# Kernel tuning notes

Measured on AMD Instinct MI355X. Metric: run time of the kernel, lower is better.

## Reference

```python
import jax, jax.numpy as jnp
import numpy as np

P = 16      # patch size
D = 768     # d_model
H = 12      # heads
L = 12      # layers
F = 3072    # d_ff
NC = 1000   # num classes
B = 32
IMG = 224
S = (IMG // P) ** 2 + 1  # 197 tokens (CLS + patches)
EPS = 1e-5


def layernorm(x, s, b):
    m = jnp.mean(x, axis=-1, keepdims=True)
    v = jnp.var(x, axis=-1, keepdims=True)
    return (x - m) * jax.lax.rsqrt(v + EPS) * s + b


def setup_inputs() -> dict:
    key = jax.random.key(0)
    ks = jax.random.split(key, 16)
    sd = 0.02
    patch_dim = P * P * 3  # 768
    inp = {
        "img": jax.random.normal(ks[0], (B, 3, IMG, IMG), jnp.float32),
        "proj_w": jax.random.normal(ks[1], (patch_dim, D), jnp.float32) * sd,
        "proj_b": jnp.zeros((D,), jnp.float32),
        "cls_token": jax.random.normal(ks[2], (1, 1, D), jnp.float32) * sd,
        "pos_emb": jax.random.normal(ks[3], (1, S, D), jnp.float32) * sd,
        # stacked per-layer params [L, ...]
        "ln1_s": jnp.ones((L, D), jnp.float32),
        "ln1_b": jnp.zeros((L, D), jnp.float32),
        "wq": jax.random.normal(ks[4], (L, D, D), jnp.float32) * sd,
        "bq": jnp.zeros((L, D), jnp.float32),
        "wk": jax.random.normal(ks[5], (L, D, D), jnp.float32) * sd,
        "bk": jnp.zeros((L, D), jnp.float32),
        "wv": jax.random.normal(ks[6], (L, D, D), jnp.float32) * sd,
        "bv": jnp.zeros((L, D), jnp.float32),
        "wo": jax.random.normal(ks[7], (L, D, D), jnp.float32) * sd,
        "bo": jnp.zeros((L, D), jnp.float32),
        "ln2_s": jnp.ones((L, D), jnp.float32),
        "ln2_b": jnp.zeros((L, D), jnp.float32),
        "w1": jax.random.normal(ks[8], (L, D, F), jnp.float32) * sd,
        "b1": jnp.zeros((L, F), jnp.float32),
        "w2": jax.random.normal(ks[9], (L, F, D), jnp.float32) * sd,
        "b2": jnp.zeros((L, D), jnp.float32),
        "fnorm_s": jnp.ones((D,), jnp.float32),
        "fnorm_b": jnp.zeros((D,), jnp.float32),
        "head_w": jax.random.normal(ks[10], (D, NC), jnp.float32) * sd,
        "head_b": jnp.zeros((NC,), jnp.float32),
    }
    return inp


def vit_forward(img, proj_w, proj_b, cls_token, pos_emb, ln1_s, ln1_b,
                wq, bq, wk, bk, wv, bv, wo, bo, ln2_s, ln2_b,
                w1, b1, w2, b2, fnorm_s, fnorm_b, head_w, head_b):
    b = img.shape[0]
    g = IMG // P
    # rearrange 'b c (h ph) (w pw) -> b (h w) (ph pw c)'
    x = img.reshape(b, 3, g, P, g, P)
    x = x.transpose(0, 2, 4, 3, 5, 1).reshape(b, g * g, P * P * 3)
    x = x @ proj_w + proj_b                      # [b, 196, D]
    cls = jnp.broadcast_to(cls_token, (b, 1, D))
    x = jnp.concatenate([cls, x], axis=1)        # [b, 197, D]
    x = x + pos_emb                              # learnable positional encoding

    dk = D // H
    scale = 1.0 / jnp.sqrt(jnp.float32(dk))

    def layer(x, p):
        (l1s, l1b, Wq, Bq, Wk, Bk, Wv, Bv, Wo, Bo,
         l2s, l2b, W1, B1, W2, B2) = p
        # pre-norm self-attention with residual
        xn = layernorm(x, l1s, l1b)
        q = (xn @ Wq + Bq).reshape(b, S, H, dk)
        k = (xn @ Wk + Bk).reshape(b, S, H, dk)
        v = (xn @ Wv + Bv).reshape(b, S, H, dk)
        scores = jnp.einsum('bqhd,bkhd->bhqk', q, k) * scale
        attn = jax.nn.softmax(scores, axis=-1)
        ao = jnp.einsum('bhqk,bkhd->bqhd', attn, v).reshape(b, S, D)
        x = x + (ao @ Wo + Bo)
        # pre-norm FFN with residual
        xn = layernorm(x, l2s, l2b)
        h = jax.nn.gelu(xn @ W1 + B1, approximate=False)
        x = x + (h @ W2 + B2)
        return x, None

    params = (ln1_s, ln1_b, wq, bq, wk, bk, wv, bv, wo, bo,
              ln2_s, ln2_b, w1, b1, w2, b2)
    x, _ = jax.lax.scan(layer, x, params)
    x = layernorm(x, fnorm_s, fnorm_b)
    cls_out = x[:, 0, :]
    return cls_out @ head_w + head_b             # [b, num_classes]


def reference(img, proj_w, proj_b, cls_token, pos_emb, ln1_s, ln1_b,
              wq, bq, wk, bk, wv, bv, wo, bo, ln2_s, ln2_b,
              w1, b1, w2, b2, fnorm_s, fnorm_b, head_w, head_b):
    return vit_forward(img, proj_w, proj_b, cls_token, pos_emb, ln1_s, ln1_b,
                       wq, bq, wk, bk, wv, bv, wo, bo, ln2_s, ln2_b,
                       w1, b1, w2, b2, fnorm_s, fnorm_b, head_w, head_b)
```

## Files before the change

### kernel.cpp

```cpp
#include <hip/hip_runtime.h>
#include <stdint.h>

typedef __attribute__((ext_vector_type(4))) float  f32x4;
typedef __attribute__((ext_vector_type(8))) _Float16 f16x8;
typedef __attribute__((ext_vector_type(8))) unsigned short u16x8;

__device__ __forceinline__ unsigned short f2h(float f) {
    _Float16 h = (_Float16)f;
    union { _Float16 h; unsigned short u; } cv; cv.h = h; return cv.u;
}

__device__ __forceinline__ f32x4 mfma16(f16x8 a, f16x8 b, f32x4 c) {
    return __builtin_amdgcn_mfma_f32_16x16x32_f16(a, b, c, 0, 0, 0);
}

__device__ __forceinline__ void async16(const unsigned short* g, unsigned short* l) {
    __builtin_amdgcn_global_load_lds(
        (const __attribute__((address_space(1))) unsigned int*)g,
        (__attribute__((address_space(3))) unsigned int*)l,
        16, 0, 0);
}

template<int EPI, int BK>
__global__ __launch_bounds__(256, (BK == 32 ? 4 : 3))
void gemm_k(const unsigned short* __restrict__ A, const unsigned short* __restrict__ Bw,
            int M, int K, int N,
            float* __restrict__ p0, unsigned short* __restrict__ p1,
            const float* __restrict__ p2, const float* __restrict__ p3,
            unsigned short* __restrict__ p4, unsigned short* __restrict__ p5)
{
    constexpr int SMSTG = 2 * 64 * BK + 2 * 128 * BK;
    constexpr int SMU   = (EPI == 0 || EPI == 2)
                          ? (SMSTG > 128 * 68 ? SMSTG : 128 * 68)
                          : SMSTG;
    __shared__ unsigned short smem[SMU];
    unsigned short (*lA)[64 * BK]  = (unsigned short(*)[64 * BK])smem;
    unsigned short (*lB)[128 * BK] = (unsigned short(*)[128 * BK])(smem + 2 * 64 * BK);
    const int tid  = threadIdx.x;
    const int lane = tid & 63;
    const int wid  = tid >> 6;

    const int gx  = gridDim.x;
    const int nwg = gx * gridDim.y;
    const int lin = blockIdx.y * gx + blockIdx.x;
    const int q = nwg >> 3, r = nwg & 7;
    const int xcd = lin & 7, i = lin >> 3;
    const int wg  = (xcd < r ? xcd * (q + 1) : r * (q + 1) + (xcd - r) * q) + i;
    const int m0 = (wg / gx) * 64;
    const int n0 = (wg % gx) * 128;

    const int colBase = wid * 32;
    const int fr = lane & 15, fg = lane >> 4;

    f32x4 acc[4][2];
#pragma unroll
    for (int a = 0; a < 4; ++a)
#pragma unroll
        for (int b = 0; b < 2; ++b) acc[a][b] = (f32x4){0.f, 0.f, 0.f, 0.f};

    const int nk = K / BK;
    constexpr int CPR = BK / 8;
    constexpr int ACH = 64 * CPR;
    constexpr int NH  = (ACH + 128 * CPR) / 256;

    auto stage = [&](int buf, int kt) {
        const int k0 = kt * BK;
#pragma unroll
        for (int h = 0; h < NH; ++h) {
            const int c = h * 256 + tid;
            const int wbase = h * 256 + wid * 64;
            if (c < ACH) {
                const int row = c / CPR, kc = c % CPR;
                const int gkc = (BK == 32) ? (kc ^ ((row >> 1) & 3)) : (kc ^ (row & 7));
                int ar = m0 + row; if (ar > M - 1) ar = M - 1;
                async16(A + (size_t)ar * K + k0 + gkc * 8,
                        &lA[buf][(size_t)wbase * 8]);
            } else {
                const int cb = c - ACH;
                const int row = cb / CPR, kc = cb % CPR;
                const int gkc = (BK == 32) ? (kc ^ ((row >> 1) & 3)) : (kc ^ (row & 7));
                async16(Bw + (size_t)(n0 + row) * K + k0 + gkc * 8,
                        &lB[buf][(size_t)(wbase - ACH) * 8]);
            }
        }
    };

    stage(0, 0);
    for (int kt = 0; kt < nk; ++kt) {
        __syncthreads();
        if (kt + 1 < nk) stage((kt + 1) & 1, kt + 1);
        const int buf = kt & 1;
#pragma unroll
        for (int kk = 0; kk < BK / 32; ++kk) {
            f16x8 af[4], bfv[2];
#pragma unroll
            for (int mi = 0; mi < 4; ++mi) {
                int row = mi * 16 + fr;
                int pc  = (BK == 32) ? (fg ^ ((row >> 1) & 3))
                                     : ((kk * 4 + fg) ^ (row & 7));
                af[mi] = *(const f16x8*)(&lA[buf][row * BK + pc * 8]);
            }
#pragma unroll
            for (int ni = 0; ni < 2; ++ni) {
                int row = colBase + ni * 16 + fr;
                int pc  = (BK == 32) ? (fg ^ ((row >> 1) & 3))
                                     : ((kk * 4 + fg) ^ (row & 7));
                bfv[ni] = *(const f16x8*)(&lB[buf][row * BK + pc * 8]);
            }
#pragma unroll
            for (int mi = 0; mi < 4; ++mi)
#pragma unroll
                for (int ni = 0; ni < 2; ++ni)
                    acc[mi][ni] = mfma16(af[mi], bfv[ni], acc[mi][ni]);
        }
    }

    const int mat0 = (EPI == 0) ? (n0 / 768) : 0;

    if constexpr (EPI == 0 || EPI == 2) {
        if (EPI == 2 || mat0 < 2) {
            unsigned short* sm = smem;
            __syncthreads();
#pragma unroll
            for (int mi = 0; mi < 4; ++mi)
#pragma unroll
                for (int ni = 0; ni < 2; ++ni) {
                    const int lcol = colBase + ni * 16 + fr;
                    const int colg = n0 + lcol;
#pragma unroll
                    for (int reg = 0; reg < 4; ++reg) {
                        const int lrow = mi * 16 + fg * 4 + reg;
                        float val = acc[mi][ni][reg] + p2[colg];
                        if (EPI == 2)
                            val = 0.5f * val * (1.0f + erff(val * 0.70710678118654752f));
                        sm[lrow * 136 + lcol] = f2h(val);
                    }
                }
            __syncthreads();
#pragma unroll
            for (int it = 0; it < 4; ++it) {
                const int e = it * 256 + tid;
                const int lrow = e >> 4, cch = e & 15;
                const int grow = m0 + lrow;
                if (grow >= M) continue;
                const u16x8 v = *(const u16x8*)(&sm[lrow * 136 + cch * 8]);
                if (EPI == 2) {
                    *(u16x8*)(p1 + (size_t)grow * 3072 + n0 + cch * 8) = v;
                } else {
                    const int colg = n0 + cch * 8;
                    const int w = colg - mat0 * 768;
                    const int h = w >> 6, d = w & 63;
                    const int b = grow / 197, s = grow - b * 197;
                    unsigned short* dst = (mat0 == 0) ? p1 : p4;
                    *(u16x8*)(dst + ((((size_t)b * 12 + h) * 197 + s) * 64 + d)) = v;
                }
            }
        } else {
            unsigned short* sm = smem;
            __syncthreads();
#pragma unroll
            for (int mi = 0; mi < 4; ++mi)
#pragma unroll
                for (int ni = 0; ni < 2; ++ni) {
                    const int lcol = colBase + ni * 16 + fr;
                    const int colg = n0 + lcol;
#pragma unroll
                    for (int reg = 0; reg < 4; ++reg) {
                        const int lrow = mi * 16 + fg * 4 + reg;
                        sm[lcol * 68 + lrow] = f2h(acc[mi][ni][reg] + p2[colg]);
                    }
                }
            __syncthreads();
            const int srow = lane;
            const int grow = m0 + srow;
            if (grow < M) {
                const int b = grow / 197, s = grow - b * 197;
#pragma unroll
                for (int it = 0; it < 32; ++it) {
                    const int c = (tid >> 6) + it * 4;
                    const int w = n0 + c - 1536;
                    const int h = w >> 6, d = w & 63;
                    p5[(((size_t)b * 12 + h) * 64 + d) * 208 + s] = sm[c * 68 + srow];
                }
            }
        }
    } else {
#pragma unroll
        for (int mi = 0; mi < 4; ++mi) {
#pragma unroll
            for (int ni = 0; ni < 2; ++ni) {
                const int col = n0 + colBase + ni * 16 + fr;
#pragma unroll
                for (int reg = 0; reg < 4; ++reg) {
                    const int row = m0 + mi * 16 + fg * 4 + reg;
                    if (row >= M) continue;
                    const float v = acc[mi][ni][reg];
                    if constexpr (EPI == 1 || EPI == 3) {
                        size_t idx = (size_t)row * 768 + col;
                        p0[idx] = p0[idx] + v + p2[col];
                    } else {
                        int b = row / 196, p = row - b * 196;
                        float val = v + p2[col] + p3[(size_t)(1 + p) * 768 + col];
                        p0[((size_t)(b * 197 + 1 + p)) * 768 + col] = val;
                    }
                }
            }
        }
    }
}

__device__ __forceinline__ void convT_body(const float* __restrict__ src,
                                           unsigned short* __restrict__ dst,
                                           int K, int N, int bx, int by,
                                           float (*t)[65])
{
    const int tid = threadIdx.x;
    const int n0 = bx * 64, k0 = by * 64;
    int r = tid >> 4, cq = tid & 15;
#pragma unroll
    for (int i = 0; i < 4; ++i) {
        f32x4 v = *(const f32x4*)(src + (size_t)(k0 + r + i * 16) * N + n0 + cq * 4);
        t[r + i * 16][cq * 4 + 0] = v.x;
        t[r + i * 16][cq * 4 + 1] = v.y;
        t[r + i * 16][cq * 4 + 2] = v.z;
        t[r + i * 16][cq * 4 + 3] = v.w;
    }
    __syncthreads();
    int nl = tid >> 2, kq = tid & 3;
    u16x8 o0, o1;
#pragma unroll
    for (int j = 0; j < 8; ++j) {
        o0[j] = f2h(t[kq * 16 + j][nl]);
        o1[j] = f2h(t[kq * 16 + 8 + j][nl]);
    }
    unsigned short* d = dst + (size_t)(n0 + nl) * K + k0 + kq * 16;
    *(u16x8*)(d)     = o0;
    *(u16x8*)(d + 8) = o1;
}

__device__ __forceinline__ void prep_block(int pid,
            const float* __restrict__ wq, const float* __restrict__ wk,
            const float* __restrict__ wv, const float* __restrict__ wo,
            const float* __restrict__ w1, const float* __restrict__ w2,
            const float* __restrict__ bq, const float* __restrict__ bk,
            const float* __restrict__ bv,
            unsigned short* __restrict__ wqkvT, unsigned short* __restrict__ woT,
            unsigned short* __restrict__ w1T, unsigned short* __restrict__ w2T,
            float* __restrict__ bqkv, float (*t)[65])
{
    if (pid == 1728) {
        for (int c = threadIdx.x; c < 2304; c += 256) {
            int m = c / 768, w = c - m * 768;
            bqkv[c] = (m == 0) ? bq[w] : (m == 1 ? bk[w] : bv[w]);
        }
        return;
    }
    const float* src; unsigned short* dst; int K, N, bx, by;
    if (pid < 576) {
        int mat = pid / 144, r = pid - mat * 144;
        K = 768; N = 768; bx = r % 12; by = r / 12;
        if (mat == 0)      { src = wq; dst = wqkvT; }
        else if (mat == 1) { src = wk; dst = wqkvT + 768ull * 768; }
        else if (mat == 2) { src = wv; dst = wqkvT + 1536ull * 768; }
        else               { src = wo; dst = woT; }
    } else if (pid < 1152) {
        int r = pid - 576; K = 768; N = 3072; bx = r % 48; by = r / 48;
        src = w1; dst = w1T;
    } else {
        int r = pid - 1152; K = 3072; N = 768; bx = r % 12; by = r / 12;
        src = w2; dst = w2T;
    }
    convT_body(src, dst, K, N, bx, by, t);
}

__global__ __launch_bounds__(256)
void prep_k(const float* __restrict__ wq, const float* __restrict__ wk,
            const float* __restrict__ wv, const float* __restrict__ wo,
            const float* __restrict__ w1, const float* __restrict__ w2,
            const float* __restrict__ bq, const float* __restrict__ bk,
            const float* __restrict__ bv,
            unsigned short* __restrict__ wqkvT, unsigned short* __restrict__ woT,
            unsigned short* __restrict__ w1T, unsigned short* __restrict__ w2T,
            float* __restrict__ bqkv)
{
    __shared__ float t[64][65];
    prep_block(blockIdx.x, wq, wk, wv, wo, w1, w2, bq, bk, bv,
               wqkvT, woT, w1T, w2T, bqkv, t);
}

__global__ __launch_bounds__(256, 4)
void attn_prep_k(const unsigned short* __restrict__ qb, const unsigned short* __restrict__ kb,
                 const unsigned short* __restrict__ vt, unsigned short* __restrict__ ao,
                 const float* __restrict__ wq, const float* __restrict__ wk,
                 const float* __restrict__ wv, const float* __restrict__ wo,
                 const float* __restrict__ w1, const float* __restrict__ w2,
                 const float* __restrict__ bq, const float* __restrict__ bk,
                 const float* __restrict__ bv,
                 unsigned short* __restrict__ wqkvT, unsigned short* __restrict__ woT,
                 unsigned short* __restrict__ w1T, unsigned short* __restrict__ w2T,
                 float* __restrict__ bqkv)
{
    __shared__ float smbuf[32 * 210 + 32];

    const int bid = blockIdx.x;
    if (bid >= 2688) {
        prep_block(bid - 2688, wq, wk, wv, wo, w1, w2, bq, bk, bv,
                   wqkvT, woT, w1T, w2T, bqkv,
                   reinterpret_cast<float(*)[65]>(smbuf));
        return;
    }

    float* sc   = smbuf;
    float* rinv = smbuf + 32 * 210;

    const int bh = bid % 384;
    const int qt = bid / 384;
    const int b = bh / 12, h = bh - b * 12;
    const unsigned short* qh  = qb + (size_t)bh * 197 * 64;
    const unsigned short* kh  = kb + (size_t)bh * 197 * 64;
    const unsigned short* vth = vt + (size_t)bh * 64 * 208;
    const int tid = threadIdx.x, lane = tid & 63, wid = tid >> 6;
    const int fr = lane & 15, fg = lane >> 4;

    f16x8 qf[2][2];
#pragma unroll
    for (int mi = 0; mi < 2; ++mi)
#pragma unroll
        for (int kc = 0; kc < 2; ++kc) {
            int s = qt * 32 + mi * 16 + fr; if (s > 196) s = 196;
            qf[mi][kc] = *(const f16x8*)(qh + (size_t)s * 64 + kc * 32 + fg * 8);
        }

    for (int nt = wid; nt < 13; nt += 4) {
        f32x4 a0 = (f32x4){0.f,0.f,0.f,0.f}, a1 = a0;
        int rs = nt * 16 + fr; if (rs > 196) rs = 196;
#pragma unroll
        for (int kc = 0; kc < 2; ++kc) {
            f16x8 kf = *(const f16x8*)(kh + (size_t)rs * 64 + kc * 32 + fg * 8);
            a0 = mfma16(qf[0][kc], kf, a0);
            a1 = mfma16(qf[1][kc], kf, a1);
        }
        int ccol = nt * 16 + fr;
        bool valid = (ccol < 197);
#pragma unroll
        for (int reg = 0; reg < 4; ++reg) {
            int mr = fg * 4 + reg;
            sc[mr * 210 + ccol]        = valid ? a0[reg] * 0.125f : -1e30f;
            sc[(16 + mr) * 210 + ccol] = valid ? a1[reg] * 0.125f : -1e30f;
        }
    }
    __syncthreads();

    {
        int row = tid >> 3, j = tid & 7;
        float m = -1e30f;
        for (int c = j; c < 208; c += 8) m = fmaxf(m, sc[row * 210 + c]);
#pragma unroll
        for (int o = 1; o < 8; o <<= 1) m = fmaxf(m, __shfl_xor(m, o));
        float sum = 0.f;
        for (int c = j; c < 208; c += 8) {
            float e = __expf(sc[row * 210 + c] - m);
            sc[row * 210 + c] = e;
            sum += e;
        }
#pragma unroll
        for (int o = 1; o < 8; o <<= 1) sum += __shfl_xor(sum, o);
        if (j == 0) rinv[row] = 1.0f / sum;
    }
    __syncthreads();

    f32x4 o0 = (f32x4){0.f,0.f,0.f,0.f}, o1 = o0;
    const int dbase = wid * 16;
    for (int kt = 0; kt < 7; ++kt) {
        int kb8 = kt * 32 + fg * 8;
        f16x8 pa0, pa1, vf;
        if (kb8 >= 208) {
#pragma unroll
            for (int j = 0; j < 8; ++j) { pa0[j] = (_Float16)0.f; pa1[j] = (_Float16)0.f; vf[j] = (_Float16)0.f; }
        } else {
            const float* pr0 = &sc[fr * 210 + kb8];
            const float* pr1 = &sc[(16 + fr) * 210 + kb8];
#pragma unroll
            for (int j = 0; j < 8; ++j) { pa0[j] = (_Float16)pr0[j]; pa1[j] = (_Float16)pr1[j]; }
            vf = *(const f16x8*)(vth + (size_t)(dbase + fr) * 208 + kb8);
        }
        o0 = mfma16(pa0, vf, o0);
        o1 = mfma16(pa1, vf, o1);
    }

    __syncthreads();
    unsigned short* ob = (unsigned short*)smbuf;
#pragma unroll
    for (int reg = 0; reg < 4; ++reg) {
        const int mr0 = fg * 4 + reg;
        ob[mr0 * 68 + dbase + fr] = f2h(o0[reg] * rinv[mr0]);
        const int mr1 = 16 + fg * 4 + reg;
        ob[mr1 * 68 + dbase + fr] = f2h(o1[reg] * rinv[mr1]);
    }
    __syncthreads();
    {
        const int rowl = tid >> 3, ch = tid & 7;
        const int s = qt * 32 + rowl;
        if (s < 197) {
            const u16x8 v = *(const u16x8*)(&ob[rowl * 68 + ch * 8]);
            *(u16x8*)(ao + ((size_t)(b * 197 + s)) * 768 + h * 64 + ch * 8) = v;
        }
    }
}

__global__ __launch_bounds__(256, 4)
void ln_k(const float* __restrict__ x, const float* __restrict__ gs,
          const float* __restrict__ gb, unsigned short* __restrict__ out)
{
    const int row = blockIdx.x;
    const int tid = threadIdx.x, lane = tid & 63, wid = tid >> 6;
    const float* xr = x + (size_t)row * 768;
    float v0 = xr[tid], v1 = xr[tid + 256], v2 = xr[tid + 512];
    float s = v0 + v1 + v2;
    float q = v0 * v0 + v1 * v1 + v2 * v2;
#pragma unroll
    for (int o = 1; o < 64; o <<= 1) { s += __shfl_xor(s, o); q += __shfl_xor(q, o); }
    __shared__ float ws[4], wq[4];
    if (lane == 0) { ws[wid] = s; wq[wid] = q; }
    __syncthreads();
    s = ws[0] + ws[1] + ws[2] + ws[3];
    q = wq[0] + wq[1] + wq[2] + wq[3];
    const float mean = s * (1.0f / 768.0f);
    const float rstd = rsqrtf(q * (1.0f / 768.0f) - mean * mean + 1e-5f);
    unsigned short* orow = out + (size_t)row * 768;
    orow[tid]       = f2h((v0 - mean) * rstd * gs[tid]       + gb[tid]);
    orow[tid + 256] = f2h((v1 - mean) * rstd * gs[tid + 256] + gb[tid + 256]);
    orow[tid + 512] = f2h((v2 - mean) * rstd * gs[tid + 512] + gb[tid + 512]);
}

__global__ __launch_bounds__(256)
void convT_k(const float* __restrict__ src, unsigned short* __restrict__ dst, int K, int N)
{
    __shared__ float t[64][65];
    convT_body(src, dst, K, N, blockIdx.x, blockIdx.y, t);
}

__global__ __launch_bounds__(256)
void patch_k(const float* __restrict__ img, unsigned short* __restrict__ patches)
{
    const int t = blockIdx.x;
    const int pxy = threadIdx.x;
    const int b = t / 196, pi = t - b * 196;
    const int gy = pi / 14, gx = pi - gy * 14;
    const int py = pxy >> 4, px = pxy & 15;
    const int yy = gy * 16 + py, xx = gx * 16 + px;
    const float* base = img + ((size_t)b * 3 * 224 + yy) * 224 + xx;
    float c0 = base[0];
    float c1 = base[224 * 224];
    float c2 = base[2 * 224 * 224];
    unsigned short* d = patches + (size_t)t * 768 + pxy * 3;
    d[0] = f2h(c0); d[1] = f2h(c1); d[2] = f2h(c2);
}

__global__ void cls_k(const float* __restrict__ cls, const float* __restrict__ pos,
                      float* __restrict__ x)
{
    int c = blockIdx.x * 256 + threadIdx.x;
    int b = blockIdx.y;
    x[((size_t)b * 197) * 768 + c] = cls[c] + pos[c];
}

__global__ __launch_bounds__(256, 4)
void head_k(const float* __restrict__ x, const float* __restrict__ fs, const float* __restrict__ fb,
            const float* __restrict__ hw, const float* __restrict__ hb, float* __restrict__ out)
{
    __shared__ float xn[768];
    __shared__ float ws[4], wq_[4];
    const int b  = blockIdx.y;
    const int n0 = blockIdx.x * 125;
    const int tid = threadIdx.x, lane = tid & 63, wid = tid >> 6;
    const float* xr = x + (size_t)b * 197 * 768;
    float v0 = xr[tid], v1 = xr[tid + 256], v2 = xr[tid + 512];
    float s = v0 + v1 + v2, q = v0 * v0 + v1 * v1 + v2 * v2;
#pragma unroll
    for (int o = 1; o < 64; o <<= 1) { s += __shfl_xor(s, o); q += __shfl_xor(q, o); }
    if (lane == 0) { ws[wid] = s; wq_[wid] = q; }
    __syncthreads();
    s = ws[0] + ws[1] + ws[2] + ws[3];
    q = wq_[0] + wq_[1] + wq_[2] + wq_[3];
    float mean = s * (1.f / 768.f);
    float rstd = rsqrtf(q * (1.f / 768.f) - mean * mean + 1e-5f);
    xn[tid]       = (v0 - mean) * rstd * fs[tid]       + fb[tid];
    xn[tid + 256] = (v1 - mean) * rstd * fs[tid + 256] + fb[tid + 256];
    xn[tid + 512] = (v2 - mean) * rstd * fs[tid + 512] + fb[tid + 512];
    __syncthreads();

    const int nrel = tid >> 1, half = tid & 1;
    const int n = n0 + nrel;
    float acc = 0.f;
    if (nrel < 125) {
        const float* hp = hw + (size_t)(half * 384) * 1000 + n;
        const float* xp = xn + half * 384;
#pragma unroll 4
        for (int k = 0; k < 384; ++k) acc = fmaf(xp[k], hp[(size_t)k * 1000], acc);
    }
    acc += __shfl_xor(acc, 1);
    if (half == 0 && nrel < 125) out[(size_t)b * 1000 + n] = acc + hb[n];
}

extern "C" void kernel_launch(void* const* d_in, const int* in_sizes, int n_in,
                              void* d_out, int out_size, void* d_ws, size_t ws_size,
                              hipStream_t stream)
{
    (void)in_sizes; (void)n_in; (void)out_size; (void)ws_size;
    const float* img    = (const float*)d_in[0];
    const float* proj_w = (const float*)d_in[1];
    const float* proj_b = (const float*)d_in[2];
    const float* cls_t  = (const float*)d_in[3];
    const float* pos    = (const float*)d_in[4];
    const float* ln1_s  = (const float*)d_in[5];
    const float* ln1_b  = (const float*)d_in[6];
    const float* wq     = (const float*)d_in[7];
    const float* bq     = (const float*)d_in[8];
    const float* wk     = (const float*)d_in[9];
    const float* bk     = (const float*)d_in[10];
    const float* wv     = (const float*)d_in[11];
    const float* bv     = (const float*)d_in[12];
    const float* wo     = (const float*)d_in[13];
    const float* bo     = (const float*)d_in[14];
    const float* ln2_s  = (const float*)d_in[15];
    const float* ln2_b  = (const float*)d_in[16];
    const float* w1     = (const float*)d_in[17];
    const float* b1     = (const float*)d_in[18];
    const float* w2     = (const float*)d_in[19];
    const float* b2     = (const float*)d_in[20];
    const float* fs     = (const float*)d_in[21];
    const float* fb     = (const float*)d_in[22];
    const float* hw     = (const float*)d_in[23];
    const float* hb     = (const float*)d_in[24];

    char* ws = (char*)d_ws;
    size_t off = 0;
    auto alloc = [&](size_t bytes) -> char* {
        char* r = ws + off;
        off += (bytes + 255) & ~(size_t)255;
        return r;
    };
    unsigned short* wqkvT[2]; unsigned short* woT[2];
    unsigned short* w1T[2];   unsigned short* w2T[2];
    float* bqkv[2];
    for (int s = 0; s < 2; ++s) {
        wqkvT[s] = (unsigned short*)alloc(2304ull * 768 * 2);
        woT[s]   = (unsigned short*)alloc(768ull * 768 * 2);
        w1T[s]   = (unsigned short*)alloc(3072ull * 768 * 2);
        w2T[s]   = (unsigned short*)alloc(768ull * 3072 * 2);
        bqkv[s]  = (float*)alloc(2304 * 4);
    }
    unsigned short* projT = (unsigned short*)alloc(768ull * 768 * 2);
    float*          x     = (float*)alloc(6304ull * 768 * 4);
    unsigned short* xn    = (unsigned short*)alloc(6304ull * 768 * 2);
    unsigned short* qbuf  = (unsigned short*)alloc(4841472ull * 2);
    unsigned short* kbuf  = (unsigned short*)alloc(4841472ull * 2);
    unsigned short* vbufT = (unsigned short*)alloc(384ull * 64 * 208 * 2);
    unsigned short* aob   = (unsigned short*)alloc(6304ull * 768 * 2);
    unsigned short* hbuf  = (unsigned short*)alloc(6304ull * 3072 * 2);
    unsigned short* patches = hbuf;

    convT_k<<<dim3(12, 12), 256, 0, stream>>>(proj_w, projT, 768, 768);
    patch_k<<<dim3(6272), 256, 0, stream>>>(img, patches);
    prep_k<<<dim3(1729), 256, 0, stream>>>(
        wq, wk, wv, wo, w1, w2, bq, bk, bv,
        wqkvT[0], woT[0], w1T[0], w2T[0], bqkv[0]);
    gemm_k<4, 32><<<dim3(6, 98), 256, 0, stream>>>(patches, projT, 6272, 768, 768,
                                                   x, nullptr, proj_b, pos, nullptr, nullptr);
    cls_k<<<dim3(3, 32), 256, 0, stream>>>(cls_t, pos, x);

    for (int l = 0; l < 12; ++l) {
        const int set = l & 1, nxt = set ^ 1;
        const int lp  = (l < 11) ? l + 1 : 11;
        const int nprep = (l < 11) ? 1729 : 0;

        ln_k<<<dim3(6304), 256, 0, stream>>>(x, ln1_s + l * 768, ln1_b + l * 768, xn);
        gemm_k<0, 32><<<dim3(18, 99), 256, 0, stream>>>(xn, wqkvT[set], 6304, 768, 2304,
                                                        nullptr, qbuf, bqkv[set], nullptr, kbuf, vbufT);
        attn_prep_k<<<dim3(2688 + nprep), 256, 0, stream>>>(
            qbuf, kbuf, vbufT, aob,
            wq + (size_t)lp * 768 * 768, wk + (size_t)lp * 768 * 768,
            wv + (size_t)lp * 768 * 768, wo + (size_t)lp * 768 * 768,
            w1 + (size_t)lp * 768 * 3072, w2 + (size_t)lp * 3072 * 768,
            bq + lp * 768, bk + lp * 768, bv + lp * 768,
            wqkvT[nxt], woT[nxt], w1T[nxt], w2T[nxt], bqkv[nxt]);
        gemm_k<1, 32><<<dim3(6, 99), 256, 0, stream>>>(aob, woT[set], 6304, 768, 768,
                                                       x, nullptr, bo + l * 768, nullptr, nullptr, nullptr);
        ln_k<<<dim3(6304), 256, 0, stream>>>(x, ln2_s + l * 768, ln2_b + l * 768, xn);
        gemm_k<2, 32><<<dim3(24, 99), 256, 0, stream>>>(xn, w1T[set], 6304, 768, 3072,
                                                        nullptr, hbuf, b1 + l * 3072, nullptr, nullptr, nullptr);
        gemm_k<3, 64><<<dim3(6, 99), 256, 0, stream>>>(hbuf, w2T[set], 6304, 3072, 768,
                                                       x, nullptr, b2 + l * 768, nullptr, nullptr, nullptr);
    }

    head_k<<<dim3(8, 32), 256, 0, stream>>>(x, fs, fb, hw, hb, (float*)d_out);
}
```

Baseline: 2.893 ms.

## Store residual stream in fp16 and stage GEMM residual epilogue through LDS

The residual activation buffer x changes from fp32 to fp16, halving its read/write traffic in the residual-add GEMM epilogues, layernorm and head kernels. The residual/patch-embed epilogues now write results into LDS first and then emit 16-byte vectorized row stores, instead of scattered scalar fp32 read-modify-writes. This costs extra LDS use and barriers in those GEMM variants. Accumulating the residual across 12 layers in fp16 may also reduce accuracy.

```diff
diff --git a/kernel.cpp b/kernel.cpp
--- a/kernel.cpp
+++ b/kernel.cpp
@@ -8,6 +8,9 @@
 __device__ __forceinline__ unsigned short f2h(float f) {
     _Float16 h = (_Float16)f;
     union { _Float16 h; unsigned short u; } cv; cv.h = h; return cv.u;
+}
+__device__ __forceinline__ float h2f(unsigned short u) {
+    union { unsigned short u; _Float16 h; } cv; cv.u = u; return (float)cv.h;
 }
 
 __device__ __forceinline__ f32x4 mfma16(f16x8 a, f16x8 b, f32x4 c) {
@@ -25,14 +28,12 @@
 __global__ __launch_bounds__(256, (BK == 32 ? 4 : 3))
 void gemm_k(const unsigned short* __restrict__ A, const unsigned short* __restrict__ Bw,
             int M, int K, int N,
-            float* __restrict__ p0, unsigned short* __restrict__ p1,
+            unsigned short* __restrict__ p0, unsigned short* __restrict__ p1,
             const float* __restrict__ p2, const float* __restrict__ p3,
             unsigned short* __restrict__ p4, unsigned short* __restrict__ p5)
 {
     constexpr int SMSTG = 2 * 64 * BK + 2 * 128 * BK;
-    constexpr int SMU   = (EPI == 0 || EPI == 2)
-                          ? (SMSTG > 128 * 68 ? SMSTG : 128 * 68)
-                          : SMSTG;
+    constexpr int SMU   = (SMSTG > 128 * 68 ? SMSTG : 128 * 68);
     __shared__ unsigned short smem[SMU];
     unsigned short (*lA)[64 * BK]  = (unsigned short(*)[64 * BK])smem;
     unsigned short (*lB)[128 * BK] = (unsigned short(*)[128 * BK])(smem + 2 * 64 * BK);
@@ -185,26 +186,46 @@
             }
         }
     } else {
-#pragma unroll
-        for (int mi = 0; mi < 4; ++mi) {
+        unsigned short* sm = smem;
+        __syncthreads();
+#pragma unroll
+        for (int mi = 0; mi < 4; ++mi)
 #pragma unroll
             for (int ni = 0; ni < 2; ++ni) {
-                const int col = n0 + colBase + ni * 16 + fr;
+                const int lcol = colBase + ni * 16 + fr;
+                const int colg = n0 + lcol;
 #pragma unroll
                 for (int reg = 0; reg < 4; ++reg) {
-                    const int row = m0 + mi * 16 + fg * 4 + reg;
-                    if (row >= M) continue;
-                    const float v = acc[mi][ni][reg];
-                    if constexpr (EPI == 1 || EPI == 3) {
-                        size_t idx = (size_t)row * 768 + col;
-                        p0[idx] = p0[idx] + v + p2[col];
+                    const int lrow = mi * 16 + fg * 4 + reg;
+                    const int grow = m0 + lrow;
+                    float val = acc[mi][ni][reg] + p2[colg];
+                    if (EPI == 4) {
+                        if (grow < M) {
+                            int b = grow / 196, p = grow - b * 196;
+                            val += p3[(size_t)(1 + p) * 768 + colg];
+                        }
                     } else {
-                        int b = row / 196, p = row - b * 196;
-                        float val = v + p2[col] + p3[(size_t)(1 + p) * 768 + col];
-                        p0[((size_t)(b * 197 + 1 + p)) * 768 + col] = val;
+                        if (grow < M) val += h2f(p0[(size_t)grow * 768 + colg]);
                     }
+                    sm[lrow * 136 + lcol] = f2h(val);
                 }
             }
+        __syncthreads();
+#pragma unroll
+        for (int it = 0; it < 4; ++it) {
+            const int e = it * 256 + tid;
+            const int lrow = e >> 4, cch = e & 15;
+            const int grow = m0 + lrow;
+            if (grow >= M) continue;
+            const u16x8 v = *(const u16x8*)(&sm[lrow * 136 + cch * 8]);
+            size_t xrow;
+            if (EPI == 4) {
+                int b = grow / 196, p = grow - b * 196;
+                xrow = (size_t)(b * 197 + 1 + p);
+            } else {
+                xrow = (size_t)grow;
+            }
+            *(u16x8*)(p0 + xrow * 768 + n0 + cch * 8) = v;
         }
     }
 }
@@ -409,13 +430,13 @@
 }
 
 __global__ __launch_bounds__(256, 4)
-void ln_k(const float* __restrict__ x, const float* __restrict__ gs,
+void ln_k(const unsigned short* __restrict__ x, const float* __restrict__ gs,
           const float* __restrict__ gb, unsigned short* __restrict__ out)
 {
     const int row = blockIdx.x;
     const int tid = threadIdx.x, lane = tid & 63, wid = tid >> 6;
-    const float* xr = x + (size_t)row * 768;
-    float v0 = xr[tid], v1 = xr[tid + 256], v2 = xr[tid + 512];
+    const unsigned short* xr = x + (size_t)row * 768;
+    float v0 = h2f(xr[tid]), v1 = h2f(xr[tid + 256]), v2 = h2f(xr[tid + 512]);
     float s = v0 + v1 + v2;
     float q = v0 * v0 + v1 * v1 + v2 * v2;
 #pragma unroll
@@ -458,15 +479,16 @@
 }
 
 __global__ void cls_k(const float* __restrict__ cls, const float* __restrict__ pos,
-                      float* __restrict__ x)
+                      unsigned short* __restrict__ x)
 {
     int c = blockIdx.x * 256 + threadIdx.x;
     int b = blockIdx.y;
-    x[((size_t)b * 197) * 768 + c] = cls[c] + pos[c];
+    x[((size_t)b * 197) * 768 + c] = f2h(cls[c] + pos[c]);
 }
 
 __global__ __launch_bounds__(256, 4)
-void head_k(const float* __restrict__ x, const float* __restrict__ fs, const float* __restrict__ fb,
+void head_k(const unsigned short* __restrict__ x, const float* __restrict__ fs,
+            const float* __restrict__ fb,
             const float* __restrict__ hw, const float* __restrict__ hb, float* __restrict__ out)
 {
     __shared__ float xn[768];
@@ -474,8 +496,8 @@
     const int b  = blockIdx.y;
     const int n0 = blockIdx.x * 125;
     const int tid = threadIdx.x, lane = tid & 63, wid = tid >> 6;
-    const float* xr = x + (size_t)b * 197 * 768;
-    float v0 = xr[tid], v1 = xr[tid + 256], v2 = xr[tid + 512];
+    const unsigned short* xr = x + (size_t)b * 197 * 768;
+    float v0 = h2f(xr[tid]), v1 = h2f(xr[tid + 256]), v2 = h2f(xr[tid + 512]);
     float s = v0 + v1 + v2, q = v0 * v0 + v1 * v1 + v2 * v2;
 #pragma unroll
     for (int o = 1; o < 64; o <<= 1) { s += __shfl_xor(s, o); q += __shfl_xor(q, o); }
@@ -552,7 +574,7 @@
         bqkv[s]  = (float*)alloc(2304 * 4);
     }
     unsigned short* projT = (unsigned short*)alloc(768ull * 768 * 2);
-    float*          x     = (float*)alloc(6304ull * 768 * 4);
+    unsigned short* x     = (unsigned short*)alloc(6304ull * 768 * 2);
     unsigned short* xn    = (unsigned short*)alloc(6304ull * 768 * 2);
     unsigned short* qbuf  = (unsigned short*)alloc(4841472ull * 2);
     unsigned short* kbuf  = (unsigned short*)alloc(4841472ull * 2);
```

Result: no change. 2.891 ms (-0.1%).
